# Optimization experiments

Hardware: AMD Instinct MI355X
Metric: run time of the kernel (lower is better)

The kernel has to match this reference:

```python
import jax, jax.numpy as jnp
import numpy as np

T = 4096; D = 768; V = 32000; L = 4; EPS = 1e-5


def _ln(x, g, b):
    m = jnp.mean(x, axis=-1, keepdims=True)
    v = jnp.mean((x - m) ** 2, axis=-1, keepdims=True)
    return (x - m) * jax.lax.rsqrt(v + EPS) * g + b


def _qgelu(x):
    return x * jax.nn.sigmoid(1.702 * x)


def setup_inputs() -> dict:
    key = jax.random.key(0)
    ks = jax.random.split(key, 10)
    s = 0.02
    return {
        "idx": jax.random.randint(ks[0], (T,), 0, V),
        "wte": jax.random.normal(ks[1], (V, D)) * s,
        "rb_ln_g": jnp.ones((D,)), "rb_ln_b": jnp.zeros((D,)),
        "rb_fc_w": jax.random.normal(ks[2], (D, 4 * D)) * s,
        "rb_fc_b": jnp.zeros((4 * D,)),
        "rb_proj_w": jax.random.normal(ks[3], (4 * D, D)) * s,
        "rb_proj_b": jnp.zeros((D,)),
        "lnf_g": jnp.ones((D,)), "lnf_b": jnp.zeros((D,)),
        "lm_head_w": jax.random.normal(ks[4], (D, V)) * s,
        "mb_ln_g": jnp.ones((L, 2 * D)), "mb_ln_b": jnp.zeros((L, 2 * D)),
        "mb_fc_w": jax.random.normal(ks[5], (L, 2 * D, 4 * D)) * s,
        "mb_fc_b": jnp.zeros((L, 4 * D)),
        "mb_proj_w": jax.random.normal(ks[6], (L, 4 * D, D)) * s,
        "mb_proj_b": jnp.zeros((L, D)),
        "op_w": jax.random.normal(ks[7], (L, D, D)) * s,
        "op_b": jnp.zeros((L, D)),
        "lns_g": jnp.ones((L, D)), "lns_b": jnp.zeros((L, D)),
        "heads_w": jax.random.normal(ks[8], (L, D, V)) * s,
    }


def reference(idx, wte, rb_ln_g, rb_ln_b, rb_fc_w, rb_fc_b, rb_proj_w, rb_proj_b,
              lnf_g, lnf_b, lm_head_w, mb_ln_g, mb_ln_b, mb_fc_w, mb_fc_b,
              mb_proj_w, mb_proj_b, op_w, op_b, lns_g, lns_b, heads_w):
    # token embedding (dropout is identity in eval) + initial residual block
    x = wte[idx]  # [T, D]
    h = _ln(x, rb_ln_g, rb_ln_b)
    x = x + _qgelu(h @ rb_fc_w + rb_fc_b) @ rb_proj_w + rb_proj_b
    x = _ln(x, lnf_g, lnf_b)
    logits = x @ lm_head_w  # [T, V]

    # targets=None path: pred_targets = cat(idx[1:], [-1])
    pred_targets = jnp.concatenate([idx[1:], jnp.full((1,), -1, idx.dtype)])
    pos = jnp.arange(T)
    skey = jax.random.key(42)

    for i in range(L):  # static small loop over layers
        j = i + 1
        # multinomial(softmax(logits), 1) == categorical(logits)
        idx_next = jax.random.categorical(jax.random.fold_in(skey, i), logits)
        # positions p where the sample matched the next-token target and p < T - j
        mask = (idx_next == pred_targets) & (pos < T - j)  # [T] bool
        # x2[p] = x[p + j] (padded); compute merge densely, select with mask
        x2 = jnp.concatenate([x[j:], jnp.zeros((j, D), x.dtype)], axis=0)
        h = _ln(jnp.concatenate([x, x2], axis=-1), mb_ln_g[i], mb_ln_b[i])
        merged = x2 + _qgelu(h @ mb_fc_w[i] + mb_fc_b[i]) @ mb_proj_w[i] + mb_proj_b[i]
        # scatter merged[p] into x at position p + j where mask[p]
        merged_s = jnp.concatenate([jnp.zeros((j, D), x.dtype), merged[:-j]], axis=0)
        mask_s = jnp.concatenate([jnp.zeros((j,), bool), mask[:-j]], axis=0)
        x = jnp.where(mask_s[:, None], merged_s, x)
        x = x @ op_w[i] + op_b[i]
        x = _ln(x, lns_g[i], lns_b[i])
        logits = x @ heads_w[i]
    return logits
```

## Files before the change

kernel.cpp:

```cpp
#include <hip/hip_runtime.h>
#include <cstdint>
#include <cstddef>

#define T_TOK 4096
#define DIM   768
#define VOCAB 32000
#define NLAYER 4
#define HALF_TV 65536000u

typedef short bf16x8 __attribute__((ext_vector_type(8)));
typedef float f32x4  __attribute__((ext_vector_type(4)));
typedef float f32x4v __attribute__((ext_vector_type(4)));

__host__ __device__ inline void tf2x32(uint32_t k0, uint32_t k1, uint32_t& v0, uint32_t& v1){
  uint32_t ks2 = k0 ^ k1 ^ 0x1BD11BDAu;
  uint32_t x0 = v0 + k0, x1 = v1 + k1;
#define TFR(R) { x0 += x1; x1 = (x1<<R)|(x1>>(32-R)); x1 ^= x0; }
  TFR(13) TFR(15) TFR(26) TFR(6)
  x0 += k1;  x1 += ks2 + 1u;
  TFR(17) TFR(29) TFR(16) TFR(24)
  x0 += ks2; x1 += k0 + 2u;
  TFR(13) TFR(15) TFR(26) TFR(6)
  x0 += k0;  x1 += k1 + 3u;
  TFR(17) TFR(29) TFR(16) TFR(24)
  x0 += k1;  x1 += ks2 + 4u;
  TFR(13) TFR(15) TFR(26) TFR(6)
  x0 += ks2; x1 += k0 + 5u;
#undef TFR
  v0 = x0; v1 = x1;
}

__device__ inline float neglog_u(uint32_t k){
  float L;
  if (k >= 0x780000u){
    float x = (float)(0x800000u - k) * 1.1920928955078125e-7f;
    L = x * fmaf(x, fmaf(x, fmaf(x, 0.25f, 0.3333333333333f), 0.5f), 1.0f);
  } else {
    float l2k = __builtin_amdgcn_logf((float)k);
    L = 0.69314718055994531f * (23.0f - l2k);
    if (k == 0u) L = 87.33654475055310898f;
  }
  return L;
}

__device__ inline void gumbel_pair(uint32_t kf0, uint32_t kf1, uint32_t t_up, uint32_t v,
                                   float& gu, float& gd){
  uint32_t m = t_up * (uint32_t)VOCAB + v;
  uint32_t x0 = m, x1 = m + HALF_TV;
  tf2x32(kf0, kf1, x0, x1);
  float Lu = neglog_u(x0 >> 9);
  float Ld = neglog_u(x1 >> 9);
  gu = -0.69314718055994531f * __builtin_amdgcn_logf(Lu);
  gd = -0.69314718055994531f * __builtin_amdgcn_logf(Ld);
}

__device__ inline unsigned short f2bf(float f){
  uint32_t u = __float_as_uint(f);
  return (unsigned short)((u + 0x7FFFu + ((u >> 16) & 1u)) >> 16);
}
__device__ inline float bf2f(unsigned short h){
  return __uint_as_float(((uint32_t)h) << 16);
}
__device__ inline void cvt8(const float* f, bool lo, unsigned short* out){
  #pragma unroll
  for (int e=0;e<8;e++){
    float x = f[e];
    unsigned short h = f2bf(x);
    if (lo) h = f2bf(x - bf2f(h));
    out[e] = h;
  }
}
__device__ inline float blockReduceSum(float v){
  __shared__ float red[4];
  #pragma unroll
  for (int off=32; off>0; off>>=1) v += __shfl_down(v, off);
  int w = threadIdx.x >> 6;
  __syncthreads();
  if ((threadIdx.x & 63) == 0) red[w] = v;
  __syncthreads();
  return red[0] + red[1] + red[2] + red[3];
}

__device__ inline void gload16(const void* g, void* l){
  __builtin_amdgcn_global_load_lds(
      (const __attribute__((address_space(1))) unsigned int*)g,
      (__attribute__((address_space(3))) unsigned int*)l, 16, 0, 0);
}

#define ASM_FENCE() asm volatile("" ::: "memory")

enum { ST_F32 = 0, ST_HILO = 1, ST_SAMPLE = 2 };

template<int KSTEPS, int NSEG, int STORE, bool NTST>
__global__ __launch_bounds__(512) void k_hgemm8(
    const unsigned short* __restrict__ A0, const unsigned short* __restrict__ A1,
    const unsigned short* __restrict__ B0, const unsigned short* __restrict__ B2,
    float* __restrict__ C, uint32_t kf0, uint32_t kf1,
    unsigned long long* __restrict__ row_best, int N)
{
  constexpr int K  = KSTEPS * 64;
  constexpr int NT = NSEG * KSTEPS;
  __shared__ unsigned short sAll[3 * 24 * 1024];

  const int t = threadIdx.x;
  const int w = t >> 6, l = t & 63;
  const int wm = w >> 1, wn = w & 1;
  const int g = l >> 4, r = l & 15;
  const int lr = l >> 3, lc = l & 7;

  int bid = blockIdx.x;
  int xcd = bid & 7, c = bid >> 3;
  int bm = xcd*2 + (c & 1);
  int bn = c >> 1;

  f32x4 acc[4][4] = {};

  size_t arow[4];
  #pragma unroll
  for (int p=0;p<4;p++){
    int mr = p*64 + w*8 + lr;
    int blk = mr >> 4;
    int grow = bm*128 + ((blk>>1)<<4) + (mr & 15) + ((blk & 1) ? 2048 : 0);
    arow[p] = (size_t)grow * K;
  }
  size_t brow[2];
  #pragma unroll
  for (int p=0;p<2;p++){
    int nr = p*64 + w*8 + lr;
    brow[p] = (size_t)(bn*128 + nr) * K;
  }
  const int swz = (lc ^ lr) << 3;
  const int ldst = (w*8)*128 + l*16;

  auto stage = [&](int vt){
    int s = vt % 3;
    int seg = (NSEG == 1) ? 0 : (vt / KSTEPS);
    int k0  = ((NSEG == 1) ? vt : (vt % KSTEPS)) * 64;
    const unsigned short* Ap = (seg == 1) ? A1 : A0;
    const unsigned short* Bp = (seg == 2) ? B2 : B0;
    char* base = (char*)sAll + s * 49152;
    #pragma unroll
    for (int p=0;p<4;p++)
      gload16(Ap + arow[p] + k0 + swz, base + p*8192 + ldst);
    char* baseB = base + 32768;
    #pragma unroll
    for (int p=0;p<2;p++)
      gload16(Bp + brow[p] + k0 + swz, baseB + p*8192 + ldst);
  };

  stage(0);
  stage(1);
  asm volatile("s_waitcnt vmcnt(6)" ::: "memory");
  ASM_FENCE(); __builtin_amdgcn_s_barrier(); ASM_FENCE();

  for (int vt = 0; vt < NT; ++vt){
    if (vt + 2 < NT) stage(vt + 2);
    if (vt + 2 < NT)      { asm volatile("s_waitcnt vmcnt(12)" ::: "memory"); }
    else if (vt + 1 < NT) { asm volatile("s_waitcnt vmcnt(6)"  ::: "memory"); }
    else                  { asm volatile("s_waitcnt vmcnt(0)"  ::: "memory"); }
    ASM_FENCE(); __builtin_amdgcn_s_barrier(); ASM_FENCE();

    const char* sA = (const char*)sAll + (vt % 3) * 49152;
    const char* sB = sA + 32768;
    #pragma unroll
    for (int kk=0;kk<2;kk++){
      bf16x8 av[4], bv[4];
      #pragma unroll
      for (int mi=0;mi<4;mi++){
        int tr = wm*64 + mi*16 + r;
        av[mi] = *(const bf16x8*)(sA + tr*128 + (((kk*4+g) ^ (r&7))<<4));
      }
      #pragma unroll
      for (int ni=0;ni<4;ni++){
        int tr = wn*64 + ni*16 + r;
        bv[ni] = *(const bf16x8*)(sB + tr*128 + (((kk*4+g) ^ (r&7))<<4));
      }
      __builtin_amdgcn_s_setprio(1);
      #pragma unroll
      for (int mi=0;mi<4;mi++)
        #pragma unroll
        for (int ni=0;ni<4;ni++)
          acc[mi][ni] = __builtin_amdgcn_mfma_f32_16x16x32_bf16(av[mi], bv[ni], acc[mi][ni], 0, 0, 0);
      __builtin_amdgcn_s_setprio(0);
    }
    ASM_FENCE(); __builtin_amdgcn_s_barrier(); ASM_FENCE();
  }

  if constexpr (STORE == ST_SAMPLE){
    #pragma unroll
    for (int mi=0; mi<4; mi+=2){
      int row16 = (wm*2 + (mi>>1)) * 16;
      #pragma unroll
      for (int jj=0;jj<4;jj++){
        uint32_t t_up = bm*128 + row16 + g*4 + jj;
        unsigned long long bu = 0ull, bd = 0ull;
        #pragma unroll
        for (int ni=0;ni<4;ni++){
          uint32_t v = bn*128 + wn*64 + ni*16 + r;
          float gu, gd;
          gumbel_pair(kf0, kf1, t_up, v, gu, gd);
          float vu = acc[mi][ni][jj]   + gu;
          float vd = acc[mi+1][ni][jj] + gd;
          uint32_t fu = __float_as_uint(vu); fu = (fu & 0x80000000u) ? ~fu : (fu | 0x80000000u);
          uint32_t fd = __float_as_uint(vd); fd = (fd & 0x80000000u) ? ~fd : (fd | 0x80000000u);
          unsigned long long pu = ((unsigned long long)fu << 32) | (unsigned long long)(~v);
          unsigned long long pd = ((unsigned long long)fd << 32) | (unsigned long long)(~v);
          if (pu > bu) bu = pu;
          if (pd > bd) bd = pd;
        }
        #pragma unroll
        for (int off=1; off<16; off<<=1){
          unsigned int l0 = (unsigned int)bu, h0 = (unsigned int)(bu>>32);
          unsigned int l1 = __shfl_xor(l0, off), h1 = __shfl_xor(h0, off);
          unsigned long long o = ((unsigned long long)h1 << 32) | (unsigned long long)l1;
          if (o > bu) bu = o;
          l0 = (unsigned int)bd; h0 = (unsigned int)(bd>>32);
          l1 = __shfl_xor(l0, off); h1 = __shfl_xor(h0, off);
          o = ((unsigned long long)h1 << 32) | (unsigned long long)l1;
          if (o > bd) bd = o;
        }
        if (r == 0){
          atomicMax(&row_best[t_up], bu);
          atomicMax(&row_best[t_up + 2048], bd);
        }
      }
    }
  } else {
    #pragma unroll
    for (int mi=0;mi<4;mi++){
      int blk2 = wm*4 + mi;
      int mbase = bm*128 + ((blk2>>1)<<4) + ((blk2 & 1) ? 2048 : 0);
      #pragma unroll
      for (int ni=0;ni<4;ni++){
        int n = bn*128 + wn*64 + ni*16 + r;
        #pragma unroll
        for (int jj=0;jj<4;jj++){
          int m = mbase + g*4 + jj;
          float v = acc[mi][ni][jj];
          if constexpr (NTST) __builtin_nontemporal_store(v, &C[(size_t)m * N + n]);
          else                C[(size_t)m * N + n] = v;
        }
      }
    }
  }
}

template<int KSTEPS, int NSEG, bool BIAS, bool QGELU, bool RES, int STORE>
__global__ __launch_bounds__(256) void k_hgemm(
    const unsigned short* __restrict__ A0, const unsigned short* __restrict__ A1,
    const unsigned short* __restrict__ B0, const unsigned short* __restrict__ B2,
    float* __restrict__ C, unsigned short* __restrict__ Ch, unsigned short* __restrict__ Cl,
    const float* __restrict__ bias, const float* __restrict__ res,
    int N, uint32_t kf0, uint32_t kf1, unsigned long long* __restrict__ row_best)
{
  constexpr int K = KSTEPS * 64;
  __shared__ unsigned short sA[128*64];
  __shared__ unsigned short sB[128*64];
  const int t = threadIdx.x;
  const int wave = t >> 6, lane = t & 63;
  const int wm = wave >> 1, wn = wave & 1;
  const int g = lane >> 4, r = lane & 15;
  const int lr = lane >> 3, lc = lane & 7;

  int bid = blockIdx.x;
  int xcd = bid & 7, c = bid >> 3;
  int bm = xcd*4 + (c & 3);
  int bn = c >> 2;

  f32x4 acc[4][4] = {};

  for (int kb = 0; kb < NSEG*KSTEPS; ++kb){
    const int seg = (NSEG == 1) ? 0 : (kb / KSTEPS);
    const int k0  = (NSEG == 1) ? kb*64 : (kb % KSTEPS) * 64;
    const unsigned short* Ap = (seg == 1) ? A1 : A0;
    const unsigned short* Bp = (seg == 2) ? B2 : B0;
    __syncthreads();
    #pragma unroll
    for (int p=0;p<4;p++){
      int mr = p*32 + wave*8 + lr;
      int blk = mr >> 4;
      int grow = bm*64 + ((blk>>1)<<4) + (mr & 15) + ((blk & 1) ? 2048 : 0);
      int gk = k0 + ((lc ^ lr) << 3);
      gload16(Ap + (size_t)grow * K + gk, (char*)sA + mr*128 + lc*16);
      int nrow = bn*128 + mr;
      gload16(Bp + (size_t)nrow * K + gk, (char*)sB + mr*128 + lc*16);
    }
    __syncthreads();
    #pragma unroll
    for (int kk=0;kk<2;kk++){
      bf16x8 av[4], bv[4];
      #pragma unroll
      for (int mi=0;mi<4;mi++){
        int tr = wm*64 + mi*16 + r;
        av[mi] = *(const bf16x8*)((const char*)sA + tr*128 + (((kk*4+g) ^ (r&7))<<4));
      }
      #pragma unroll
      for (int ni=0;ni<4;ni++){
        int tr = wn*64 + ni*16 + r;
        bv[ni] = *(const bf16x8*)((const char*)sB + tr*128 + (((kk*4+g) ^ (r&7))<<4));
      }
      #pragma unroll
      for (int mi=0;mi<4;mi++)
        #pragma unroll
        for (int ni=0;ni<4;ni++)
          acc[mi][ni] = __builtin_amdgcn_mfma_f32_16x16x32_bf16(av[mi], bv[ni], acc[mi][ni], 0, 0, 0);
    }
  }

  #pragma unroll
  for (int mi=0;mi<4;mi++){
    int blk2 = wm*4 + mi;
    int mbase = bm*64 + ((blk2>>1)<<4) + ((blk2 & 1) ? 2048 : 0);
    #pragma unroll
    for (int ni=0;ni<4;ni++){
      int n = bn*128 + wn*64 + ni*16 + r;
      float bv_ = BIAS ? bias[n] : 0.0f;
      #pragma unroll
      for (int jj=0;jj<4;jj++){
        int m = mbase + g*4 + jj;
        float v = acc[mi][ni][jj] + bv_;
        if constexpr (QGELU) v = v / (1.0f + expf(-1.702f * v));
        if constexpr (RES)   v += res[(size_t)m * N + n];
        if constexpr (STORE == ST_F32){
          C[(size_t)m * N + n] = v;
        } else {
          unsigned short h = f2bf(v);
          Ch[(size_t)m * N + n] = h;
          Cl[(size_t)m * N + n] = f2bf(v - bf2f(h));
        }
      }
    }
  }
}

template<bool SPLIT>
__global__ __launch_bounds__(256) void k_wt_t(const float* __restrict__ W,
    unsigned short* __restrict__ Bh, unsigned short* __restrict__ Bl, int K, int N)
{
  __shared__ unsigned short sH[64][72];
  __shared__ unsigned short sL[64][72];
  int kt = blockIdx.x, nt = blockIdx.y;
  int t = threadIdx.x;
  int kr = t >> 4, nc4 = (t & 15) * 4;
  #pragma unroll
  for (int p=0;p<4;p++){
    int k = p*16 + kr;
    f32x4v w = __builtin_nontemporal_load((const f32x4v*)&W[(size_t)(kt*64 + k) * N + nt*64 + nc4]);
    #pragma unroll
    for (int e=0;e<4;e++){
      unsigned short h = f2bf(w[e]);
      sH[nc4+e][k] = h;
      if (SPLIT) sL[nc4+e][k] = f2bf(w[e] - bf2f(h));
    }
  }
  __syncthreads();
  #pragma unroll
  for (int q=0;q<2;q++){
    int cid = t + q*256;
    int n = cid >> 3, ch = cid & 7;
    *(bf16x8*)&Bh[(size_t)(nt*64+n)*K + kt*64 + ch*8] = *(const bf16x8*)&sH[n][ch*8];
    if (SPLIT)
      *(bf16x8*)&Bl[(size_t)(nt*64+n)*K + kt*64 + ch*8] = *(const bf16x8*)&sL[n][ch*8];
  }
}

__global__ __launch_bounds__(256) void k_embed_ln(const int* __restrict__ idx,
    const float* __restrict__ wte, const float* __restrict__ g, const float* __restrict__ b,
    float* __restrict__ Xraw, unsigned short* __restrict__ Hh, unsigned short* __restrict__ Hl)
{
  int row = blockIdx.x;
  const float* src = wte + (size_t)idx[row] * DIM;
  float v[3];
  #pragma unroll
  for (int jj=0;jj<3;jj++) v[jj] = src[threadIdx.x + jj*256];
  float s = blockReduceSum(v[0]+v[1]+v[2]);
  float mean = s * (1.0f/DIM);
  float s2 = 0;
  #pragma unroll
  for (int jj=0;jj<3;jj++){ float d = v[jj]-mean; s2 += d*d; }
  s2 = blockReduceSum(s2);
  float rs = rsqrtf(s2 * (1.0f/DIM) + 1e-5f);
  #pragma unroll
  for (int jj=0;jj<3;jj++){
    int d = threadIdx.x + jj*256;
    Xraw[(size_t)row*DIM + d] = v[jj];
    float o = (v[jj]-mean)*rs*g[d] + b[d];
    unsigned short h = f2bf(o);
    Hh[(size_t)row*DIM + d] = h;
    Hl[(size_t)row*DIM + d] = f2bf(o - bf2f(h));
  }
}

__global__ __launch_bounds__(256) void k_ln(const float* __restrict__ in, float* __restrict__ out,
    const float* __restrict__ g, const float* __restrict__ b,
    unsigned short* __restrict__ obf, unsigned short* __restrict__ olo)
{
  int row = blockIdx.x;
  const float* src = in + (size_t)row * DIM;
  float v[3];
  #pragma unroll
  for (int jj=0;jj<3;jj++) v[jj] = src[threadIdx.x + jj*256];
  float s = blockReduceSum(v[0]+v[1]+v[2]);
  float mean = s * (1.0f/DIM);
  float s2 = 0;
  #pragma unroll
  for (int jj=0;jj<3;jj++){ float d = v[jj]-mean; s2 += d*d; }
  s2 = blockReduceSum(s2);
  float rs = rsqrtf(s2 * (1.0f/DIM) + 1e-5f);
  #pragma unroll
  for (int jj=0;jj<3;jj++){
    int d = threadIdx.x + jj*256;
    float o = (v[jj]-mean)*rs*g[d] + b[d];
    out[(size_t)row*DIM + d] = o;
    unsigned short h = f2bf(o);
    obf[(size_t)row*DIM + d] = h;
    olo[(size_t)row*DIM + d] = f2bf(o - bf2f(h));
  }
}

__global__ void k_mask(const unsigned long long* __restrict__ row_best,
    const int* __restrict__ idx, int j, int* __restrict__ count, int* __restrict__ plist)
{
  int t = blockIdx.x * blockDim.x + threadIdx.x;
  if (t >= T_TOK) return;
  int v = (int)(~(uint32_t)(row_best[t] & 0xFFFFFFFFull));
  int tgt = (t < T_TOK-1) ? idx[t+1] : -1;
  if (v == tgt && t < T_TOK - j){
    int pos = atomicAdd(count, 1);
    plist[pos] = t;
  }
}

__global__ __launch_bounds__(256) void k_merge(const float* __restrict__ X,
    const int* __restrict__ plist, const int* __restrict__ count,
    const float* __restrict__ lng, const float* __restrict__ lnb,
    const float* __restrict__ fcw, const float* __restrict__ fcb,
    const float* __restrict__ pjw, const float* __restrict__ pjb,
    float* __restrict__ mergebuf, int j)
{
  __shared__ float sh[1536 + 3072];
  int nb = *count;
  for (int bIdx = blockIdx.x; bIdx < nb; bIdx += gridDim.x){
    int p = plist[bIdx];
    const float* xp = X + (size_t)p * DIM;
    const float* x2 = X + (size_t)(p + j) * DIM;
    for (int d = threadIdx.x; d < 1536; d += 256)
      sh[d] = (d < DIM) ? xp[d] : x2[d - DIM];
    __syncthreads();
    float s = 0;
    for (int d = threadIdx.x; d < 1536; d += 256) s += sh[d];
    s = blockReduceSum(s);
    float mean = s * (1.0f/1536.0f);
    float s2 = 0;
    for (int d = threadIdx.x; d < 1536; d += 256){ float df = sh[d]-mean; s2 += df*df; }
    s2 = blockReduceSum(s2);
    float rs = rsqrtf(s2 * (1.0f/1536.0f) + 1e-5f);
    __syncthreads();
    for (int d = threadIdx.x; d < 1536; d += 256)
      sh[d] = (sh[d]-mean)*rs*lng[d] + lnb[d];
    __syncthreads();
    float* act = sh + 1536;
    #pragma unroll
    for (int jj=0;jj<12;jj++){
      int n = threadIdx.x + jj*256;
      float a = fcb[n];
      for (int k=0;k<1536;k++) a += sh[k]*fcw[(size_t)k*3072 + n];
      act[n] = a / (1.0f + expf(-1.702f*a));
    }
    __syncthreads();
    #pragma unroll
    for (int jj=0;jj<3;jj++){
      int d = threadIdx.x + jj*256;
      float a = pjb[d];
      for (int k=0;k<3072;k++) a += act[k]*pjw[(size_t)k*DIM + d];
      mergebuf[(size_t)bIdx*DIM + d] = x2[d] + a;
    }
    __syncthreads();
  }
}

__global__ void k_scatter(float* __restrict__ X, unsigned short* __restrict__ Xbf,
    unsigned short* __restrict__ Xlo, const float* __restrict__ mergebuf,
    const int* __restrict__ plist, const int* __restrict__ count, int j)
{
  int nb = *count;
  for (int bIdx = blockIdx.x; bIdx < nb; bIdx += gridDim.x){
    int p = plist[bIdx];
    for (int d = threadIdx.x; d < DIM; d += 256){
      float v = mergebuf[(size_t)bIdx*DIM + d];
      size_t o = (size_t)(p + j)*DIM + d;
      X[o] = v;
      unsigned short h = f2bf(v);
      Xbf[o] = h;
      Xlo[o] = f2bf(v - bf2f(h));
    }
  }
}

__global__ __launch_bounds__(256) void k_gemm_old(
    const float* __restrict__ A, const float* __restrict__ B, float* __restrict__ C,
    int M, int N, int K)
{
  __shared__ unsigned short sA[128*64];
  __shared__ unsigned short sB[128*64];
  const int t = threadIdx.x;
  const int bn = blockIdx.x, bm = blockIdx.y;
  const int wave = t >> 6, lane = t & 63;
  const int wm = wave >> 1, wn = wave & 1;
  const int g = lane >> 4, r = lane & 15;
  f32x4 acc[4][4] = {};
  const int nK = K >> 6;
  const int aC = t & 7,  aM0 = t >> 3;
  const int bN0 = t & 31, bC = t >> 5;
  const float* Abase = A + (size_t)(bm*128) * K;
  const float* Bbase = B + (size_t)(bn*128);
  for (int seg = 0; seg < 3; ++seg) {
    const bool aLO = (seg == 1), bLO = (seg == 2);
    for (int kb = 0; kb < nK; ++kb) {
      const int k0 = kb << 6;
      __syncthreads();
      #pragma unroll
      for (int p=0;p<4;p++){
        int m = p*32 + aM0;
        const float* src = Abase + (size_t)m * K + k0 + aC*8;
        float ff[8];
        *(float4*)(ff)   = *(const float4*)(src);
        *(float4*)(ff+4) = *(const float4*)(src+4);
        unsigned short hh[8];
        cvt8(ff, aLO, hh);
        *(bf16x8*)&sA[m*64 + ((aC ^ (m & 7)) * 8)] = *(bf16x8*)hh;
      }
      #pragma unroll
      for (int p=0;p<4;p++){
        int n = p*32 + bN0;
        float ff[8];
        const float* src = Bbase + (size_t)(k0 + bC*8) * N + n;
        #pragma unroll
        for (int e=0;e<8;e++) ff[e] = src[(size_t)e * N];
        unsigned short hh[8];
        cvt8(ff, bLO, hh);
        *(bf16x8*)&sB[n*64 + ((bC ^ (n & 7)) * 8)] = *(bf16x8*)hh;
      }
      __syncthreads();
      #pragma unroll
      for (int kk=0;kk<2;kk++){
        bf16x8 av[4], bv[4];
        #pragma unroll
        for (int mi=0;mi<4;mi++){
          int m = wm*64 + mi*16 + r;
          av[mi] = *(const bf16x8*)&sA[m*64 + (((kk*4 + g) ^ (m & 7)) * 8)];
        }
        #pragma unroll
        for (int ni=0;ni<4;ni++){
          int n = wn*64 + ni*16 + r;
          bv[ni] = *(const bf16x8*)&sB[n*64 + (((kk*4 + g) ^ (n & 7)) * 8)];
        }
        #pragma unroll
        for (int mi=0;mi<4;mi++)
          #pragma unroll
          for (int ni=0;ni<4;ni++)
            acc[mi][ni] = __builtin_amdgcn_mfma_f32_16x16x32_bf16(av[mi], bv[ni], acc[mi][ni], 0, 0, 0);
      }
    }
  }
  #pragma unroll
  for (int mi=0;mi<4;mi++)
    #pragma unroll
    for (int ni=0;ni<4;ni++)
      #pragma unroll
      for (int jj=0;jj<4;jj++){
        int m = bm*128 + wm*64 + mi*16 + g*4 + jj;
        int n = bn*128 + wn*64 + ni*16 + r;
        C[(size_t)m * N + n] = acc[mi][ni][jj];
      }
}

static void fold_key(uint32_t i, uint32_t& o0, uint32_t& o1){
  uint32_t x0 = 0, x1 = i;
  tf2x32(0u, 42u, x0, x1);
  o0 = x0; o1 = x1;
}

extern "C" void kernel_launch(void* const* d_in, const int* in_sizes, int n_in,
                              void* d_out, int out_size, void* d_ws, size_t ws_size,
                              hipStream_t stream)
{
  const int*   idx       = (const int*)  d_in[0];
  const float* wte       = (const float*)d_in[1];
  const float* rb_ln_g   = (const float*)d_in[2];
  const float* rb_ln_b   = (const float*)d_in[3];
  const float* rb_fc_w   = (const float*)d_in[4];
  const float* rb_fc_b   = (const float*)d_in[5];
  const float* rb_proj_w = (const float*)d_in[6];
  const float* rb_proj_b = (const float*)d_in[7];
  const float* lnf_g     = (const float*)d_in[8];
  const float* lnf_b     = (const float*)d_in[9];
  const float* lm_head_w = (const float*)d_in[10];
  const float* mb_ln_g   = (const float*)d_in[11];
  const float* mb_ln_b   = (const float*)d_in[12];
  const float* mb_fc_w   = (const float*)d_in[13];
  const float* mb_fc_b   = (const float*)d_in[14];
  const float* mb_proj_w = (const float*)d_in[15];
  const float* mb_proj_b = (const float*)d_in[16];
  const float* op_w      = (const float*)d_in[17];
  const float* op_b      = (const float*)d_in[18];
  const float* lns_g     = (const float*)d_in[19];
  const float* lns_b     = (const float*)d_in[20];
  const float* heads_w   = (const float*)d_in[21];

  const size_t TD = (size_t)T_TOK * DIM;
  const size_t DV = (size_t)DIM * VOCAB;

  float* X = (float*)d_ws;
  float* Y = X + TD;
  unsigned short* Xbf = (unsigned short*)(Y + TD);
  unsigned short* Xlo = Xbf + TD;
  unsigned short* BtFh = Xlo + TD;
  unsigned short* BtFl = BtFh + DV;
  size_t need_big = (size_t)((char*)(BtFl + DV) - (char*)d_ws);
  bool big = ws_size >= need_big;

  char* ob = (char*)d_out;
  float* OUT = (float*)d_out;
  unsigned short* Hh     = (unsigned short*)(ob);
  unsigned short* Hl     = Hh + TD;
  unsigned short* ACTh   = (unsigned short*)(ob + ((size_t)16<<20));
  unsigned short* ACTl   = ACTh + TD*4;
  unsigned short* Btfc_h = (unsigned short*)(ob + ((size_t)72<<20));
  unsigned short* Btfc_l = Btfc_h + (size_t)3072*DIM;
  unsigned short* Btpj_h = (unsigned short*)(ob + ((size_t)84<<20));
  unsigned short* Btpj_l = Btpj_h + (size_t)3072*DIM;
  unsigned short* BtS    = (unsigned short*)(ob + ((size_t)96<<20));
  unsigned short* Btop_h = (unsigned short*)(ob + ((size_t)152<<20));
  unsigned short* Btop_l = Btop_h + (size_t)DIM*DIM;
  float* MERGE = (float*)(ob + ((size_t)160<<20));
  unsigned long long* ROWBEST = (unsigned long long*)(ob + ((size_t)176<<20));
  int* PLIST = (int*)(ROWBEST + T_TOK);
  int* COUNT = PLIST + T_TOK;

  dim3 blk(256);
  dim3 blk8(512);

  k_embed_ln<<<T_TOK, blk, 0, stream>>>(idx, wte, rb_ln_g, rb_ln_b, X, Hh, Hl);
  k_wt_t<true><<<dim3(12,48), blk, 0, stream>>>(rb_fc_w,   Btfc_h, Btfc_l, DIM,  3072);
  k_wt_t<true><<<dim3(48,12), blk, 0, stream>>>(rb_proj_w, Btpj_h, Btpj_l, 3072, DIM);
  k_hgemm<12,3,true,true,false,ST_HILO><<<24*32, blk, 0, stream>>>(
      Hh, Hl, Btfc_h, Btfc_l, nullptr, ACTh, ACTl, rb_fc_b, nullptr, 3072, 0u,0u, nullptr);
  k_hgemm<48,3,true,false,true,ST_F32><<<6*32, blk, 0, stream>>>(
      ACTh, ACTl, Btpj_h, Btpj_l, Y, nullptr, nullptr, rb_proj_b, X, DIM, 0u,0u, nullptr);
  k_ln<<<T_TOK, blk, 0, stream>>>(Y, X, lnf_g, lnf_b, Xbf, Xlo);

  for (int i = 0; i < NLAYER; ++i){
    int j = i + 1;
    uint32_t kf0, kf1; fold_key((uint32_t)i, kf0, kf1);

    hipMemsetAsync(ROWBEST, 0, (size_t)T_TOK*8, stream);
    hipMemsetAsync(COUNT, 0, 4, stream);

    const float* hw = (i == 0) ? lm_head_w : heads_w + (size_t)(i-1)*DV;
    k_wt_t<false><<<dim3(12,500), blk, 0, stream>>>(hw, BtS, nullptr, DIM, VOCAB);
    k_hgemm8<12,1,ST_SAMPLE,false><<<4000, blk8, 0, stream>>>(
        Xbf, Xbf, BtS, BtS, nullptr, kf0, kf1, ROWBEST, VOCAB);

    k_mask<<<T_TOK/256, blk, 0, stream>>>(ROWBEST, idx, j, COUNT, PLIST);
    k_merge<<<64, blk, 0, stream>>>(X, PLIST, COUNT,
        mb_ln_g + (size_t)i*1536, mb_ln_b + (size_t)i*1536,
        mb_fc_w + (size_t)i*1536*3072, mb_fc_b + (size_t)i*3072,
        mb_proj_w + (size_t)i*3072*DIM, mb_proj_b + (size_t)i*DIM, MERGE, j);
    k_scatter<<<64, blk, 0, stream>>>(X, Xbf, Xlo, MERGE, PLIST, COUNT, j);

    k_wt_t<true><<<dim3(12,12), blk, 0, stream>>>(op_w + (size_t)i*DIM*DIM, Btop_h, Btop_l, DIM, DIM);
    k_hgemm<12,3,true,false,false,ST_F32><<<6*32, blk, 0, stream>>>(
        Xbf, Xlo, Btop_h, Btop_l, Y, nullptr, nullptr, op_b + (size_t)i*DIM, nullptr,
        DIM, 0u,0u, nullptr);
    k_ln<<<T_TOK, blk, 0, stream>>>(Y, X, lns_g + (size_t)i*DIM, lns_b + (size_t)i*DIM, Xbf, Xlo);
  }

  if (big){
    k_wt_t<true><<<dim3(12,500), blk, 0, stream>>>(heads_w + (size_t)3*DV, BtFh, BtFl, DIM, VOCAB);
    k_hgemm8<12,3,ST_F32,true><<<4000, blk8, 0, stream>>>(
        Xbf, Xlo, BtFh, BtFl, OUT, 0u, 0u, nullptr, VOCAB);
  } else {
    k_gemm_old<<<dim3(VOCAB/128, T_TOK/128), blk, 0, stream>>>(
        X, heads_w + (size_t)3*DV, OUT, T_TOK, VOCAB, DIM);
  }
}
```

Baseline: 3.114 ms.

## Interleave split prefetch halves with MFMA compute in bf16 GEMM main loop

Splits each tile's global-to-LDS prefetch into two halves and issues each half inside its k-substep, after the LDS fragment reads and before the MFMA block. The wait-then-barrier sequence moves from the top of the loop to the end of the second substep, and extra barriers are added between substeps. The aim is to spread memory issue across compute and reduce stalls at the loop head. The compiler memory fences around barriers are removed, which adds some risk that LDS accesses get reordered across barriers.

```diff
diff --git a/kernel.cpp b/kernel.cpp
--- a/kernel.cpp
+++ b/kernel.cpp
@@ -87,8 +87,6 @@
       (__attribute__((address_space(3))) unsigned int*)l, 16, 0, 0);
 }
 
-#define ASM_FENCE() asm volatile("" ::: "memory")
-
 enum { ST_F32 = 0, ST_HILO = 1, ST_SAMPLE = 2 };
 
 template<int KSTEPS, int NSEG, int STORE, bool NTST>
@@ -132,36 +130,34 @@
   const int swz = (lc ^ lr) << 3;
   const int ldst = (w*8)*128 + l*16;
 
-  auto stage = [&](int vt){
+  auto stage_half = [&](int vt, int half){
     int s = vt % 3;
     int seg = (NSEG == 1) ? 0 : (vt / KSTEPS);
     int k0  = ((NSEG == 1) ? vt : (vt % KSTEPS)) * 64;
     const unsigned short* Ap = (seg == 1) ? A1 : A0;
     const unsigned short* Bp = (seg == 2) ? B2 : B0;
     char* base = (char*)sAll + s * 49152;
-    #pragma unroll
-    for (int p=0;p<4;p++)
-      gload16(Ap + arow[p] + k0 + swz, base + p*8192 + ldst);
-    char* baseB = base + 32768;
-    #pragma unroll
-    for (int p=0;p<2;p++)
-      gload16(Bp + brow[p] + k0 + swz, baseB + p*8192 + ldst);
+    if (half == 0){
+      gload16(Ap + arow[0] + k0 + swz, base + 0*8192 + ldst);
+      gload16(Ap + arow[1] + k0 + swz, base + 1*8192 + ldst);
+      gload16(Ap + arow[2] + k0 + swz, base + 2*8192 + ldst);
+    } else {
+      gload16(Ap + arow[3] + k0 + swz, base + 3*8192 + ldst);
+      gload16(Bp + brow[0] + k0 + swz, base + 32768 + 0*8192 + ldst);
+      gload16(Bp + brow[1] + k0 + swz, base + 32768 + 1*8192 + ldst);
+    }
   };
 
-  stage(0);
-  stage(1);
+  stage_half(0,0); stage_half(0,1);
+  stage_half(1,0); stage_half(1,1);
   asm volatile("s_waitcnt vmcnt(6)" ::: "memory");
-  ASM_FENCE(); __builtin_amdgcn_s_barrier(); ASM_FENCE();
+  __builtin_amdgcn_s_barrier();
 
   for (int vt = 0; vt < NT; ++vt){
-    if (vt + 2 < NT) stage(vt + 2);
-    if (vt + 2 < NT)      { asm volatile("s_waitcnt vmcnt(12)" ::: "memory"); }
-    else if (vt + 1 < NT) { asm volatile("s_waitcnt vmcnt(6)"  ::: "memory"); }
-    else                  { asm volatile("s_waitcnt vmcnt(0)"  ::: "memory"); }
-    ASM_FENCE(); __builtin_amdgcn_s_barrier(); ASM_FENCE();
-
     const char* sA = (const char*)sAll + (vt % 3) * 49152;
     const char* sB = sA + 32768;
+    const bool pre = (vt + 2 < NT);
+
     #pragma unroll
     for (int kk=0;kk<2;kk++){
       bf16x8 av[4], bv[4];
@@ -175,6 +171,8 @@
         int tr = wn*64 + ni*16 + r;
         bv[ni] = *(const bf16x8*)(sB + tr*128 + (((kk*4+g) ^ (r&7))<<4));
       }
+      if (pre) stage_half(vt+2, kk);
+      __builtin_amdgcn_s_barrier();
       __builtin_amdgcn_s_setprio(1);
       #pragma unroll
       for (int mi=0;mi<4;mi++)
@@ -182,8 +180,16 @@
         for (int ni=0;ni<4;ni++)
           acc[mi][ni] = __builtin_amdgcn_mfma_f32_16x16x32_bf16(av[mi], bv[ni], acc[mi][ni], 0, 0, 0);
       __builtin_amdgcn_s_setprio(0);
-    }
-    ASM_FENCE(); __builtin_amdgcn_s_barrier(); ASM_FENCE();
+      if (kk == 0){
+        __builtin_amdgcn_s_barrier();
+      } else {
+        if (vt + 1 < NT){
+          if (pre) { asm volatile("s_waitcnt vmcnt(6)" ::: "memory"); }
+          else     { asm volatile("s_waitcnt vmcnt(0)" ::: "memory"); }
+        }
+        __builtin_amdgcn_s_barrier();
+      }
+    }
   }
 
   if constexpr (STORE == ST_SAMPLE){
```

After: 2.948 ms. -5.4%, faster.

## Widen vocab GEMM tile to 256x256 with double-buffered LDS pipeline

Applied to the files above, without the earlier changes.

The big vocab GEMM kernel now computes a 256x256 output tile per 512-thread block: 2 wave rows by 4 wave columns, each wave holding 8x4 accumulator fragments. This halves the grid to 2000 blocks and raises operand reuse per loaded tile. The LDS pipeline drops from three stages with explicit vmcnt waits to two 64KB stages guarded by __syncthreads, so less load latency is hidden. The larger accumulator array raises register pressure, and 128KB of LDS per block limits occupancy.

```diff
diff --git a/kernel.cpp b/kernel.cpp
--- a/kernel.cpp
+++ b/kernel.cpp
@@ -87,12 +87,10 @@
       (__attribute__((address_space(3))) unsigned int*)l, 16, 0, 0);
 }
 
-#define ASM_FENCE() asm volatile("" ::: "memory")
-
 enum { ST_F32 = 0, ST_HILO = 1, ST_SAMPLE = 2 };
 
 template<int KSTEPS, int NSEG, int STORE, bool NTST>
-__global__ __launch_bounds__(512) void k_hgemm8(
+__global__ __launch_bounds__(512) void k_hgemm256(
     const unsigned short* __restrict__ A0, const unsigned short* __restrict__ A1,
     const unsigned short* __restrict__ B0, const unsigned short* __restrict__ B2,
     float* __restrict__ C, uint32_t kf0, uint32_t kf1,
@@ -100,11 +98,11 @@
 {
   constexpr int K  = KSTEPS * 64;
   constexpr int NT = NSEG * KSTEPS;
-  __shared__ unsigned short sAll[3 * 24 * 1024];
+  __shared__ unsigned short sAll[65536];
 
   const int t = threadIdx.x;
   const int w = t >> 6, l = t & 63;
-  const int wm = w >> 1, wn = w & 1;
+  const int wm = w >> 2, wn = w & 3;
   const int g = l >> 4, r = l & 15;
   const int lr = l >> 3, lc = l & 7;
 
@@ -113,90 +111,84 @@
   int bm = xcd*2 + (c & 1);
   int bn = c >> 1;
 
-  f32x4 acc[4][4] = {};
-
-  size_t arow[4];
+  f32x4 acc[8][4] = {};
+
+  int grow[8];
   #pragma unroll
   for (int p=0;p<4;p++){
     int mr = p*64 + w*8 + lr;
     int blk = mr >> 4;
-    int grow = bm*128 + ((blk>>1)<<4) + (mr & 15) + ((blk & 1) ? 2048 : 0);
-    arow[p] = (size_t)grow * K;
-  }
-  size_t brow[2];
-  #pragma unroll
-  for (int p=0;p<2;p++){
+    grow[p] = (bm*128 + ((blk>>1)<<4) + (mr & 15) + ((blk & 1) ? 2048 : 0)) * K;
+  }
+  #pragma unroll
+  for (int p=0;p<4;p++){
     int nr = p*64 + w*8 + lr;
-    brow[p] = (size_t)(bn*128 + nr) * K;
-  }
-  const int swz = (lc ^ lr) << 3;
-  const int ldst = (w*8)*128 + l*16;
+    grow[4+p] = (bn*256 + nr) * K;
+  }
+  const int swz  = (lc ^ lr) << 3;
+  const int ldst = w*1024 + l*16;
 
   auto stage = [&](int vt){
-    int s = vt % 3;
+    char* base = (char*)sAll + (vt & 1) * 65536;
     int seg = (NSEG == 1) ? 0 : (vt / KSTEPS);
     int k0  = ((NSEG == 1) ? vt : (vt % KSTEPS)) * 64;
     const unsigned short* Ap = (seg == 1) ? A1 : A0;
     const unsigned short* Bp = (seg == 2) ? B2 : B0;
-    char* base = (char*)sAll + s * 49152;
     #pragma unroll
     for (int p=0;p<4;p++)
-      gload16(Ap + arow[p] + k0 + swz, base + p*8192 + ldst);
-    char* baseB = base + 32768;
-    #pragma unroll
-    for (int p=0;p<2;p++)
-      gload16(Bp + brow[p] + k0 + swz, baseB + p*8192 + ldst);
+      gload16(Ap + (size_t)(grow[p] + k0) + swz, base + p*8192 + ldst);
+    #pragma unroll
+    for (int p=0;p<4;p++)
+      gload16(Bp + (size_t)(grow[4+p] + k0) + swz, base + 32768 + p*8192 + ldst);
   };
 
   stage(0);
-  stage(1);
-  asm volatile("s_waitcnt vmcnt(6)" ::: "memory");
-  ASM_FENCE(); __builtin_amdgcn_s_barrier(); ASM_FENCE();
+  __syncthreads();
 
   for (int vt = 0; vt < NT; ++vt){
-    if (vt + 2 < NT) stage(vt + 2);
-    if (vt + 2 < NT)      { asm volatile("s_waitcnt vmcnt(12)" ::: "memory"); }
-    else if (vt + 1 < NT) { asm volatile("s_waitcnt vmcnt(6)"  ::: "memory"); }
-    else                  { asm volatile("s_waitcnt vmcnt(0)"  ::: "memory"); }
-    ASM_FENCE(); __builtin_amdgcn_s_barrier(); ASM_FENCE();
-
-    const char* sA = (const char*)sAll + (vt % 3) * 49152;
+    if (vt + 1 < NT) stage(vt + 1);
+    const char* sA = (const char*)sAll + (vt & 1) * 65536;
     const char* sB = sA + 32768;
+    __builtin_amdgcn_s_setprio(1);
     #pragma unroll
     for (int kk=0;kk<2;kk++){
-      bf16x8 av[4], bv[4];
-      #pragma unroll
-      for (int mi=0;mi<4;mi++){
-        int tr = wm*64 + mi*16 + r;
-        av[mi] = *(const bf16x8*)(sA + tr*128 + (((kk*4+g) ^ (r&7))<<4));
-      }
+      bf16x8 bv[4];
       #pragma unroll
       for (int ni=0;ni<4;ni++){
         int tr = wn*64 + ni*16 + r;
         bv[ni] = *(const bf16x8*)(sB + tr*128 + (((kk*4+g) ^ (r&7))<<4));
       }
-      __builtin_amdgcn_s_setprio(1);
-      #pragma unroll
-      for (int mi=0;mi<4;mi++)
-        #pragma unroll
-        for (int ni=0;ni<4;ni++)
-          acc[mi][ni] = __builtin_amdgcn_mfma_f32_16x16x32_bf16(av[mi], bv[ni], acc[mi][ni], 0, 0, 0);
-      __builtin_amdgcn_s_setprio(0);
-    }
-    ASM_FENCE(); __builtin_amdgcn_s_barrier(); ASM_FENCE();
+      #pragma unroll
+      for (int mh=0; mh<2; mh++){
+        bf16x8 av[4];
+        #pragma unroll
+        for (int q=0;q<4;q++){
+          int tr = wm*128 + (mh*4+q)*16 + r;
+          av[q] = *(const bf16x8*)(sA + tr*128 + (((kk*4+g) ^ (r&7))<<4));
+        }
+        #pragma unroll
+        for (int q=0;q<4;q++)
+          #pragma unroll
+          for (int ni=0;ni<4;ni++)
+            acc[mh*4+q][ni] = __builtin_amdgcn_mfma_f32_16x16x32_bf16(av[q], bv[ni], acc[mh*4+q][ni], 0, 0, 0);
+      }
+    }
+    __builtin_amdgcn_s_setprio(0);
+    __syncthreads();
   }
 
   if constexpr (STORE == ST_SAMPLE){
     #pragma unroll
-    for (int mi=0; mi<4; mi+=2){
-      int row16 = (wm*2 + (mi>>1)) * 16;
+    for (int mi=0; mi<8; mi+=2){
+      int blk = wm*8 + mi;
+      int row16 = (blk>>1) << 4;
       #pragma unroll
       for (int jj=0;jj<4;jj++){
         uint32_t t_up = bm*128 + row16 + g*4 + jj;
         unsigned long long bu = 0ull, bd = 0ull;
         #pragma unroll
         for (int ni=0;ni<4;ni++){
-          uint32_t v = bn*128 + wn*64 + ni*16 + r;
+          uint32_t v = bn*256 + wn*64 + ni*16 + r;
           float gu, gd;
           gumbel_pair(kf0, kf1, t_up, v, gu, gd);
           float vu = acc[mi][ni][jj]   + gu;
@@ -227,12 +219,12 @@
     }
   } else {
     #pragma unroll
-    for (int mi=0;mi<4;mi++){
-      int blk2 = wm*4 + mi;
-      int mbase = bm*128 + ((blk2>>1)<<4) + ((blk2 & 1) ? 2048 : 0);
+    for (int mi=0;mi<8;mi++){
+      int blk = wm*8 + mi;
+      int mbase = bm*128 + ((blk>>1)<<4) + ((blk & 1) ? 2048 : 0);
       #pragma unroll
       for (int ni=0;ni<4;ni++){
-        int n = bn*128 + wn*64 + ni*16 + r;
+        int n = bn*256 + wn*64 + ni*16 + r;
         #pragma unroll
         for (int jj=0;jj<4;jj++){
           int m = mbase + g*4 + jj;
@@ -659,7 +651,7 @@
 
     const float* hw = (i == 0) ? lm_head_w : heads_w + (size_t)(i-1)*DV;
     k_wt_t<false><<<dim3(12,500), blk, 0, stream>>>(hw, BtS, nullptr, DIM, VOCAB);
-    k_hgemm8<12,1,ST_SAMPLE,false><<<4000, blk8, 0, stream>>>(
+    k_hgemm256<12,1,ST_SAMPLE,false><<<2000, blk8, 0, stream>>>(
         Xbf, Xbf, BtS, BtS, nullptr, kf0, kf1, ROWBEST, VOCAB);
 
     k_mask<<<T_TOK/256, blk, 0, stream>>>(ROWBEST, idx, j, COUNT, PLIST);
@@ -678,7 +670,7 @@
 
   if (big){
     k_wt_t<true><<<dim3(12,500), blk, 0, stream>>>(heads_w + (size_t)3*DV, BtFh, BtFl, DIM, VOCAB);
-    k_hgemm8<12,3,ST_F32,true><<<4000, blk8, 0, stream>>>(
+    k_hgemm256<12,3,ST_F32,true><<<2000, blk8, 0, stream>>>(
         Xbf, Xlo, BtFh, BtFl, OUT, 0u, 0u, nullptr, VOCAB);
   } else {
     k_gemm_old<<<dim3(VOCAB/128, T_TOK/128), blk, 0, stream>>>(
```

After: 2.814 ms. -9.7%, faster.
